# Optimization experiments

Hardware: AMD Instinct MI355X
Metric: run time of the kernel (lower is better)

The kernel has to match this reference:

```python
import jax, jax.numpy as jnp
import numpy as np

L = 248      # max_clip_seq_len
WIN = 3      # window_size
H = 8        # attention heads
D = 768      # input/output dim
HID = 256    # rope hidden dim
SIGMA = 2.0
EPS_LN = 1e-5


def _layernorm(x, g, b):
    m = jnp.mean(x, axis=-1, keepdims=True)
    v = jnp.var(x, axis=-1, keepdims=True)
    return (x - m) / jnp.sqrt(v + EPS_LN) * g + b


def _normalize(x):
    n = jnp.linalg.norm(x, axis=-1, keepdims=True)
    return x / jnp.maximum(n, 1e-12)


def _peb_forward(word_feat, text_feat_full, word_pos, ctx_W, ctx_b, in_W, in_b,
                 out_W, out_b, cn_g, cn_b, r1_W, r1_b, ln_g, ln_b, r2_W, r2_b,
                 pos_emb, pos_temp):
    B, N, _ = word_feat.shape
    valid = word_pos != -1                              # [B,N] bool
    vf = valid.astype(word_feat.dtype)[..., None]       # [B,N,1]
    wp = jnp.clip(word_pos, 0, L - 1)                   # [B,N]
    half = WIN // 2
    offs = jnp.arange(-half, half + 1)
    positions = jnp.clip(wp[..., None] + offs[None, None, :], 0, L - 1)
    ctx = text_feat_full[jnp.arange(B)[:, None, None], positions]
    ctx_anchor = (ctx.reshape(B, N, WIN * D) @ ctx_W + ctx_b) * vf       # [B,N,D]
    q = word_feat * vf                                  # word_proj is Identity (768->768)
    # MultiheadAttention (batch_first), query=q, key=value=ctx_anchor
    hd = D // H
    qp = (q @ in_W[:, :D] + in_b[:D]).reshape(B, N, H, hd)
    kp = (ctx_anchor @ in_W[:, D:2 * D] + in_b[D:2 * D]).reshape(B, N, H, hd)
    vp = (ctx_anchor @ in_W[:, 2 * D:] + in_b[2 * D:]).reshape(B, N, H, hd)
    scores = jnp.einsum('bqhd,bkhd->bhqk', qp, kp) / jnp.sqrt(jnp.asarray(hd, q.dtype))
    attn = jax.nn.softmax(scores, axis=-1)
    ao = jnp.einsum('bhqk,bkhd->bqhd', attn, vp).reshape(B, N, D)
    attn_out = ao @ out_W + out_b
    x = _layernorm(q + attn_out, cn_g, cn_b) * vf       # word_feat_with_ctx
    # rope_mapping: Linear -> GELU -> LayerNorm -> Linear
    rope = _layernorm(jax.nn.gelu(x @ r1_W + r1_b, approximate=False), ln_g, ln_b) @ r2_W + r2_b
    rope_n = _normalize(rope)
    clip_ref_n = _normalize(pos_emb)                    # [L,D]
    temp = jnp.maximum(pos_temp, 0.001)
    logits = jnp.einsum('bnd,ld->bnl', rope_n, clip_ref_n) / temp
    log_q = jax.nn.log_softmax(logits, axis=-1)
    # gaussian soft target over L positions
    pos_idx = jnp.arange(L, dtype=jnp.float32)
    d2 = (pos_idx[None, None, :] - wp[..., None].astype(jnp.float32)) ** 2
    targ = jnp.exp(-d2 / (2.0 * SIGMA ** 2))
    targ = targ / (targ.sum(axis=-1, keepdims=True) + 1e-12)
    lqv = log_q * vf
    tv = targ * vf
    n_valid = valid.sum().astype(jnp.float32)
    safe_t = jnp.where(tv > 0, tv, 1.0)
    kl = jnp.sum(jnp.where(tv > 0, tv * (jnp.log(safe_t) - lqv), 0.0)) / (n_valid + 1e-12)
    # relative position loss on cosine similarity
    pos_sim01 = (jnp.einsum('bnd,bmd->bnm', rope_n, rope_n) + 1.0) / 2.0
    wpf = wp.astype(jnp.float32)
    target_sim = 1.0 - jnp.abs(wpf[:, :, None] - wpf[:, None, :]) / float(L)
    vm2 = vf[:, :, 0][:, None, :] * vf[:, :, 0][:, :, None]
    rel = jnp.sum((pos_sim01 * vm2 - target_sim * vm2) ** 2) / (vm2.sum() + 1e-12)
    peb_loss = (1.0 * kl + 0.5 * rel) * 1.0             # kl_weight=1, rel_weight=0.5, peb_weight=1
    # scatter blended positional features to 248-length sequence (vectorized over batch)
    vals = 0.8 * pos_emb[wp] + 0.2 * rope               # [B,N,D]
    pos_s = jnp.where(valid, wp, L)                     # invalid -> OOB index, dropped
    emb = jnp.zeros((B, L, D), word_feat.dtype).at[jnp.arange(B)[:, None], pos_s].set(vals, mode='drop')
    return emb, peb_loss, kl, rel


def setup_inputs() -> dict:
    key = jax.random.key(0)
    ks = jax.random.split(key, 20)
    B, N = 128, 128
    word_feat = jax.random.normal(ks[0], (B, N, D), jnp.float32)
    text_feat_full = jax.random.normal(ks[1], (B, L, D), jnp.float32)
    # unique sorted positions per batch (scatter is then deterministic, matching torch)
    perms = jax.vmap(lambda k: jax.random.permutation(k, L))(jax.random.split(ks[2], B))
    word_pos = jnp.sort(perms[:, :N], axis=-1).astype(jnp.int32)
    s = 0.02
    return {
        'word_feat': word_feat,
        'text_feat_full': text_feat_full,
        'word_pos': word_pos,
        'ctx_W': s * jax.random.normal(ks[3], (WIN * D, D), jnp.float32),
        'ctx_b': s * jax.random.normal(ks[4], (D,), jnp.float32),
        'in_W': s * jax.random.normal(ks[5], (D, 3 * D), jnp.float32),
        'in_b': s * jax.random.normal(ks[6], (3 * D,), jnp.float32),
        'out_W': s * jax.random.normal(ks[7], (D, D), jnp.float32),
        'out_b': s * jax.random.normal(ks[8], (D,), jnp.float32),
        'cn_g': jnp.ones((D,), jnp.float32) + s * jax.random.normal(ks[9], (D,), jnp.float32),
        'cn_b': s * jax.random.normal(ks[10], (D,), jnp.float32),
        'r1_W': s * jax.random.normal(ks[11], (D, HID), jnp.float32),
        'r1_b': s * jax.random.normal(ks[12], (HID,), jnp.float32),
        'ln_g': jnp.ones((HID,), jnp.float32) + s * jax.random.normal(ks[13], (HID,), jnp.float32),
        'ln_b': s * jax.random.normal(ks[14], (HID,), jnp.float32),
        'r2_W': s * jax.random.normal(ks[15], (HID, D), jnp.float32),
        'r2_b': s * jax.random.normal(ks[16], (D,), jnp.float32),
        'pos_emb': jax.random.normal(ks[17], (L, D), jnp.float32),
        'pos_temp': jnp.asarray(1.0, jnp.float32),
    }


def reference(word_feat, text_feat_full, word_pos, ctx_W, ctx_b, in_W, in_b,
              out_W, out_b, cn_g, cn_b, r1_W, r1_b, ln_g, ln_b, r2_W, r2_b,
              pos_emb, pos_temp):
    return _peb_forward(word_feat, text_feat_full, word_pos, ctx_W, ctx_b, in_W, in_b,
                        out_W, out_b, cn_g, cn_b, r1_W, r1_b, ln_g, ln_b, r2_W, r2_b,
                        pos_emb, pos_temp)
```

## Files before the change

### kernel.cpp

```cpp
#include <hip/hip_runtime.h>
#include <math.h>

#define BB   128
#define NN   128
#define LL   248
#define DD   768
#define HH   8
#define HDh  96
#define HIDN 256
#define MROWS (BB*NN)
#define MB_   (1u<<20)
#define KVLD 1536

typedef unsigned short u16;
typedef unsigned int   u32;
typedef __attribute__((ext_vector_type(8))) short s16x8;
typedef __attribute__((ext_vector_type(4))) float f32x4;

__device__ __forceinline__ u16 f2bf(float x) {
    u32 u = __float_as_uint(x);
    u32 r = u + 0x7fffu + ((u >> 16) & 1u);
    return (u16)(r >> 16);
}
__device__ __forceinline__ float bf2f(u16 h) {
    return __uint_as_float(((u32)h) << 16);
}
__device__ __forceinline__ void gload16(const void* g, void* l) {
    __builtin_amdgcn_global_load_lds(
        (const __attribute__((address_space(1))) void*)g,
        (__attribute__((address_space(3))) void*)l, 16, 0, 0);
}

template<int NT>
__device__ __forceinline__ float breduce_sum(float v, float* red) {
    const int tid = threadIdx.x;
    red[tid] = v; __syncthreads();
#pragma unroll
    for (int o = NT / 2; o > 0; o >>= 1) {
        if (tid < o) red[tid] += red[tid + o];
        __syncthreads();
    }
    float r = red[0]; __syncthreads();
    return r;
}
__device__ __forceinline__ double breduce_sum_d256(double v, double* red) {
    const int tid = threadIdx.x;
    red[tid] = v; __syncthreads();
#pragma unroll
    for (int o = 128; o > 0; o >>= 1) {
        if (tid < o) red[tid] += red[tid + o];
        __syncthreads();
    }
    double r = red[0]; __syncthreads();
    return r;
}

__global__ __launch_bounds__(256)
void transposeAll_kernel(const float* __restrict__ ctx_W, u16* __restrict__ ctx_Wt,
                         const float* __restrict__ in_W,  u16* __restrict__ in_Wt,
                         const float* __restrict__ out_W, u16* __restrict__ out_Wt,
                         const float* __restrict__ r1_W,  u16* __restrict__ r1_Wt,
                         const float* __restrict__ r2_W,  u16* __restrict__ r2_Wt) {
    __shared__ float t[32][33];
    int bid = blockIdx.x;
    const float* src; u16* dst; int R, C;
    if (bid < 1728)      { src = ctx_W; dst = ctx_Wt; R = 2304; C = 768;  }
    else if (bid < 3456) { src = in_W;  dst = in_Wt;  R = 768;  C = 2304; bid -= 1728; }
    else if (bid < 4032) { src = out_W; dst = out_Wt; R = 768;  C = 768;  bid -= 3456; }
    else if (bid < 4224) { src = r1_W;  dst = r1_Wt;  R = 768;  C = 256;  bid -= 4032; }
    else                 { src = r2_W;  dst = r2_Wt;  R = 256;  C = 768;  bid -= 4224; }
    const int ct = C >> 5;
    const int r0 = (bid / ct) * 32, c0 = (bid % ct) * 32;
    const int tx = threadIdx.x & 31, ty = threadIdx.x >> 5;
#pragma unroll
    for (int i = 0; i < 32; i += 8)
        t[ty + i][tx] = src[(size_t)(r0 + ty + i) * C + c0 + tx];
    __syncthreads();
#pragma unroll
    for (int i = 0; i < 32; i += 8)
        dst[(size_t)(c0 + ty + i) * R + r0 + tx] = f2bf(t[tx][ty + i]);
}

#define TEXT_N8 (BB*LL*DD/8)
#define Q_N8    (MROWS*(DD/8))
__global__ __launch_bounds__(256)
void prep_elem_kernel(const float* __restrict__ text, u16* __restrict__ textb,
                      const float* __restrict__ wf, u16* __restrict__ qb,
                      const int* __restrict__ wpos, int* __restrict__ cpos) {
    const int TOT = TEXT_N8 + Q_N8 + MROWS;
    int i = blockIdx.x * 256 + threadIdx.x;
    const int stride = gridDim.x * 256;
    for (; i < TOT; i += stride) {
        if (i < TEXT_N8) {
            const float4* s = (const float4*)(text + (size_t)i * 8);
            float4 a = s[0], b = s[1];
            uint4 o;
            o.x = (u32)f2bf(a.x) | ((u32)f2bf(a.y) << 16);
            o.y = (u32)f2bf(a.z) | ((u32)f2bf(a.w) << 16);
            o.z = (u32)f2bf(b.x) | ((u32)f2bf(b.y) << 16);
            o.w = (u32)f2bf(b.z) | ((u32)f2bf(b.w) << 16);
            *(uint4*)(textb + (size_t)i * 8) = o;
        } else if (i < TEXT_N8 + Q_N8) {
            int c = i - TEXT_N8;
            int row = c / 96;
            float vf = (wpos[row] != -1) ? 1.f : 0.f;
            const float4* s = (const float4*)(wf + (size_t)c * 8);
            float4 a = s[0], b = s[1];
            uint4 o;
            o.x = (u32)f2bf(a.x * vf) | ((u32)f2bf(a.y * vf) << 16);
            o.y = (u32)f2bf(a.z * vf) | ((u32)f2bf(a.w * vf) << 16);
            o.z = (u32)f2bf(b.x * vf) | ((u32)f2bf(b.y * vf) << 16);
            o.w = (u32)f2bf(b.z * vf) | ((u32)f2bf(b.w * vf) << 16);
            *(uint4*)(qb + (size_t)c * 8) = o;
        } else {
            int r = i - TEXT_N8 - Q_N8;
            int w = wpos[r];
            cpos[r] = w < 0 ? 0 : (w > LL - 1 ? LL - 1 : w);
        }
    }
}

__global__ __launch_bounds__(256)
void clipb_kernel(const float* __restrict__ pe, u16* __restrict__ clipb) {
    __shared__ float red[256];
    const int l = blockIdx.x, tid = threadIdx.x;
    if (l >= LL) {
        for (int j = 0; j < 3; ++j)
            clipb[(size_t)l * DD + tid + j * 256] = 0;
        return;
    }
    float t[3]; float q = 0.f;
#pragma unroll
    for (int j = 0; j < 3; ++j) {
        t[j] = pe[(size_t)l * DD + tid + j * 256];
        q = fmaf(t[j], t[j], q);
    }
    q = breduce_sum<256>(q, red);
    float inv = 1.f / fmaxf(sqrtf(q), 1e-12f);
#pragma unroll
    for (int j = 0; j < 3; ++j)
        clipb[(size_t)l * DD + tid + j * 256] = f2bf(t[j] * inv);
}

__device__ __forceinline__ void gemm_step(
    const u16* ga0, const u16* ga1, const u16* gb0, const u16* gb1,
    u16* Ad0, u16* Ad1, u16* Bd0, u16* Bd1,
    const u16* Alds, const u16* Blds,
    const int* aoff, const int* boff, f32x4 acc[4][4]) {
    gload16(ga0, Ad0); gload16(ga1, Ad1);
    gload16(gb0, Bd0); gload16(gb1, Bd1);
    __syncthreads();
    s16x8 af[4], bf[4];
#pragma unroll
    for (int m = 0; m < 4; ++m) af[m] = *(const s16x8*)(Alds + aoff[m]);
#pragma unroll
    for (int n = 0; n < 4; ++n) bf[n] = *(const s16x8*)(Blds + boff[n]);
#pragma unroll
    for (int m = 0; m < 4; ++m)
#pragma unroll
        for (int n = 0; n < 4; ++n)
            acc[m][n] = __builtin_amdgcn_mfma_f32_16x16x32_bf16(
                af[m], bf[n], acc[m][n], 0, 0, 0);
    __syncthreads();
}

template<int GATHER, int CBF16, int MASK>
__global__ __launch_bounds__(256)
void gemm_bt(const u16* __restrict__ A,
             const u16* __restrict__ TXT,
             const int* __restrict__ cpos,
             const u16* __restrict__ Bt,
             const float* __restrict__ bias,
             void* __restrict__ Cout, int ldc, int K,
             const int* __restrict__ wpos) {
    __shared__ __align__(16) u16 Alds[128 * 32];
    __shared__ __align__(16) u16 Blds[128 * 32];
    const int tid = threadIdx.x;
    const int l = tid & 63, wv = tid >> 6;

    const int gx  = gridDim.x;
    const int hw  = blockIdx.y * gx + blockIdx.x;
    const int nwg = gx * gridDim.y;
    const int cpx = nwg >> 3;
    const int lin = (hw & 7) * cpx + (hw >> 3);
    const int m0 = (lin / gx) * 128, n0 = (lin % gx) * 128;

    const int f0 = wv * 1024 + l * 16;
    const int f1 = f0 + 4096;
    const int rA0 = f0 >> 6, rA1 = f1 >> 6;
    const int cb0 = (f0 & 63) ^ (((rA0 >> 1) & 3) << 4);
    const int cb1 = (f1 & 63) ^ (((rA1 >> 1) & 3) << 4);
    const int c0e = cb0 >> 1, c1e = cb1 >> 1;

    u16* Ad0 = Alds + wv * 512;
    u16* Ad1 = Alds + 2048 + wv * 512;
    u16* Bd0 = Blds + wv * 512;
    u16* Bd1 = Blds + 2048 + wv * 512;

    const u16* pb0 = Bt + (size_t)(n0 + rA0) * K + c0e;
    const u16* pb1 = Bt + (size_t)(n0 + rA1) * K + c1e;

    const int wm = (wv >> 1) * 64, wn = (wv & 1) * 64;
    const int la = l & 15, lg = l >> 4;

    int aoff[4], boff[4];
#pragma unroll
    for (int m = 0; m < 4; ++m) {
        int ra = wm + m * 16 + la;
        aoff[m] = ra * 32 + ((lg * 8) ^ (((ra >> 1) & 3) << 3));
        int rb = wn + m * 16 + la;
        boff[m] = rb * 32 + ((lg * 8) ^ (((rb >> 1) & 3) << 3));
    }

    f32x4 acc[4][4] = {};

    if constexpr (GATHER) {
        const int g0 = m0 + rA0, g1 = m0 + rA1;
        const int gb0 = g0 >> 7, gb1 = g1 >> 7;
        const int gc0 = cpos[g0], gc1 = cpos[g1];
#pragma unroll 1
        for (int w = 0; w < 3; ++w) {
            int p0 = gc0 + w - 1; p0 = p0 < 0 ? 0 : (p0 > LL - 1 ? LL - 1 : p0);
            int p1 = gc1 + w - 1; p1 = p1 < 0 ? 0 : (p1 > LL - 1 ? LL - 1 : p1);
            const u16* a0 = TXT + ((size_t)(gb0 * LL + p0)) * DD + c0e;
            const u16* a1 = TXT + ((size_t)(gb1 * LL + p1)) * DD + c1e;
            const u16* b0 = pb0 + w * DD;
            const u16* b1 = pb1 + w * DD;
#pragma unroll 1
            for (int kt = 0; kt < 24; ++kt)
                gemm_step(a0 + kt * 32, a1 + kt * 32, b0 + kt * 32, b1 + kt * 32,
                          Ad0, Ad1, Bd0, Bd1, Alds, Blds, aoff, boff, acc);
        }
    } else {
        const u16* pa0 = A + (size_t)(m0 + rA0) * K + c0e;
        const u16* pa1 = A + (size_t)(m0 + rA1) * K + c1e;
        const int nk = K >> 5;
#pragma unroll 1
        for (int kt = 0; kt < nk; ++kt)
            gemm_step(pa0 + (kt << 5), pa1 + (kt << 5), pb0 + (kt << 5), pb1 + (kt << 5),
                      Ad0, Ad1, Bd0, Bd1, Alds, Blds, aoff, boff, acc);
    }

#pragma unroll
    for (int m = 0; m < 4; ++m) {
        const int rb = m0 + wm + m * 16 + lg * 4;
        float vf[4];
        if constexpr (MASK) {
#pragma unroll
            for (int r = 0; r < 4; ++r) vf[r] = (wpos[rb + r] != -1) ? 1.f : 0.f;
        }
#pragma unroll
        for (int n = 0; n < 4; ++n) {
            const int col = n0 + wn + n * 16 + la;
            const float bv = bias[col];
#pragma unroll
            for (int r = 0; r < 4; ++r) {
                float o = acc[m][n][r] + bv;
                if constexpr (MASK) o *= vf[r];
                if constexpr (CBF16)
                    ((u16*)Cout)[(size_t)(rb + r) * ldc + col] = f2bf(o);
                else
                    ((float*)Cout)[(size_t)(rb + r) * ldc + col] = o;
            }
        }
    }
}

__global__ __launch_bounds__(512)
void attn_mfma_kernel(const u16* __restrict__ qp, const u16* __restrict__ kvb,
                      u16* __restrict__ ao) {
    __shared__ __align__(16) u16 K_lds[128 * 96];
    __shared__ __align__(16) u16 Vt_lds[96 * 128];
    __shared__ __align__(16) u16 P_lds[128 * 128];
    const int bh = blockIdx.x;
    const int b = bh >> 3, h = bh & 7;
    const int tid = threadIdx.x;
    const int l = tid & 63, wv = tid >> 6;
    const int la = l & 15, lg = l >> 4;
    const float scale = 0.10206207261596575f;

    const size_t qbase  = ((size_t)b * NN) * DD + h * HDh;
    const size_t kvbase = ((size_t)b * NN) * KVLD + h * HDh;

#pragma unroll
    for (int i = 0; i < 3; ++i) {
        int f = i * 8192 + wv * 1024 + l * 16;
        int row = f / 192;
        int inner = f - row * 192;
        gload16((const char*)(kvb + kvbase + (size_t)row * KVLD) + inner,
                (char*)K_lds + f);
    }

    uint4 vchunk[3]; int vkey[3], vd0[3];
#pragma unroll
    for (int i = 0; i < 3; ++i) {
        int c = tid + i * 512;
        int key = c / 12, dc = c - key * 12;
        vkey[i] = key; vd0[i] = dc * 8;
        vchunk[i] = *(const uint4*)(kvb + kvbase + (size_t)key * KVLD + DD + dc * 8);
    }

    const int q0 = wv * 16;
    s16x8 qf[3];
#pragma unroll
    for (int kt = 0; kt < 3; ++kt)
        qf[kt] = *(const s16x8*)(qp + qbase + (size_t)(q0 + la) * DD + kt * 32 + lg * 8);

#pragma unroll
    for (int i = 0; i < 3; ++i) {
        const u16* e = (const u16*)&vchunk[i];
#pragma unroll
        for (int j = 0; j < 8; ++j) {
            int d = vd0[i] + j;
            int byte = ((d * 128 + vkey[i]) * 2) ^ ((d & 7) << 4);
            *(u16*)((char*)Vt_lds + byte) = e[j];
        }
    }
    __syncthreads();

    f32x4 sacc[8] = {};
#pragma unroll
    for (int kt = 0; kt < 3; ++kt) {
#pragma unroll
        for (int nf = 0; nf < 8; ++nf) {
            s16x8 bfr = *(const s16x8*)(K_lds + (nf * 16 + la) * 96 + kt * 32 + lg * 8);
            sacc[nf] = __builtin_amdgcn_mfma_f32_16x16x32_bf16(qf[kt], bfr, sacc[nf], 0, 0, 0);
        }
    }

#pragma unroll
    for (int r = 0; r < 4; ++r) {
        float m = -1e30f;
#pragma unroll
        for (int nf = 0; nf < 8; ++nf) m = fmaxf(m, sacc[nf][r]);
#pragma unroll
        for (int o = 8; o > 0; o >>= 1) m = fmaxf(m, __shfl_xor(m, o, 64));
        m *= scale;
        float p[8]; float s = 0.f;
#pragma unroll
        for (int nf = 0; nf < 8; ++nf) { p[nf] = expf(sacc[nf][r] * scale - m); s += p[nf]; }
#pragma unroll
        for (int o = 8; o > 0; o >>= 1) s += __shfl_xor(s, o, 64);
        const float inv = 1.f / s;
        const int q = q0 + lg * 4 + r;
#pragma unroll
        for (int nf = 0; nf < 8; ++nf) {
            int byte = ((q * 128 + nf * 16 + la) * 2) ^ ((q & 7) << 4);
            *(u16*)((char*)P_lds + byte) = f2bf(p[nf] * inv);
        }
    }
    __syncthreads();

    f32x4 oacc[6] = {};
#pragma unroll
    for (int kk = 0; kk < 4; ++kk) {
        const int qrow = q0 + la;
        int abyte = ((qrow * 128 + kk * 32 + lg * 8) * 2) ^ ((qrow & 7) << 4);
        s16x8 af = *(const s16x8*)((char*)P_lds + abyte);
#pragma unroll
        for (int nf = 0; nf < 6; ++nf) {
            const int d = nf * 16 + la;
            int bbyte = ((d * 128 + kk * 32 + lg * 8) * 2) ^ ((d & 7) << 4);
            s16x8 bfr = *(const s16x8*)((char*)Vt_lds + bbyte);
            oacc[nf] = __builtin_amdgcn_mfma_f32_16x16x32_bf16(af, bfr, oacc[nf], 0, 0, 0);
        }
    }

#pragma unroll
    for (int nf = 0; nf < 6; ++nf) {
#pragma unroll
        for (int r = 0; r < 4; ++r) {
            const int q = q0 + lg * 4 + r;
            ao[qbase + (size_t)q * DD + nf * 16 + la] = f2bf(oacc[nf][r]);
        }
    }
}

__global__ __launch_bounds__(256)
void ln768_kernel(const u16* __restrict__ qb, const u16* __restrict__ at,
                  const int* __restrict__ wpos, const float* __restrict__ g,
                  const float* __restrict__ bta, u16* __restrict__ xout) {
    __shared__ float red[256];
    const int r = blockIdx.x, tid = threadIdx.x;
    const float vf = (wpos[r] != -1) ? 1.f : 0.f;
    float t[3]; float s = 0.f, q = 0.f;
#pragma unroll
    for (int j = 0; j < 3; ++j) {
        int d = tid + j * 256;
        t[j] = bf2f(qb[(size_t)r * DD + d]) + bf2f(at[(size_t)r * DD + d]);
        s += t[j];
        q = fmaf(t[j], t[j], q);
    }
    s = breduce_sum<256>(s, red);
    q = breduce_sum<256>(q, red);
    float mean = s * (1.f / DD);
    float var  = q * (1.f / DD) - mean * mean;
    float inv  = 1.f / sqrtf(var + 1e-5f);
#pragma unroll
    for (int j = 0; j < 3; ++j) {
        int d = tid + j * 256;
        xout[(size_t)r * DD + d] = f2bf(((t[j] - mean) * inv * g[d] + bta[d]) * vf);
    }
}

__global__ __launch_bounds__(256)
void ln256_gelu_kernel(const float* __restrict__ g1, const float* __restrict__ lg,
                       const float* __restrict__ lb, u16* __restrict__ hout) {
    __shared__ float red[256];
    const int r = blockIdx.x, tid = threadIdx.x;
    float v  = g1[(size_t)r * HIDN + tid];
    float ge = 0.5f * v * (1.f + erff(v * 0.7071067811865475f));
    float s = breduce_sum<256>(ge, red);
    float q = breduce_sum<256>(ge * ge, red);
    float mean = s * (1.f / HIDN);
    float var  = q * (1.f / HIDN) - mean * mean;
    float inv  = 1.f / sqrtf(var + 1e-5f);
    hout[(size_t)r * HIDN + tid] = f2bf((ge - mean) * inv * lg[tid] + lb[tid]);
}

__global__ __launch_bounds__(256)
void norm_scatter_kernel(const u16* __restrict__ ropeb, const float* __restrict__ pe,
                         const int* __restrict__ wpos, u16* __restrict__ rnb,
                         float* __restrict__ emb) {
    __shared__ float red[256];
    const int r = blockIdx.x, tid = threadIdx.x;
    float t[3]; float q = 0.f;
#pragma unroll
    for (int j = 0; j < 3; ++j) {
        t[j] = bf2f(ropeb[(size_t)r * DD + tid + j * 256]);
        q = fmaf(t[j], t[j], q);
    }
    q = breduce_sum<256>(q, red);
    float inv = 1.f / fmaxf(sqrtf(q), 1e-12f);
    const int wr = wpos[r];
    const bool valid = (wr != -1);
    const int wp = wr < 0 ? 0 : (wr > LL - 1 ? LL - 1 : wr);
    const int b = r >> 7;
#pragma unroll
    for (int j = 0; j < 3; ++j) {
        int d = tid + j * 256;
        rnb[(size_t)r * DD + d] = f2bf(t[j] * inv);
        if (valid)
            emb[((size_t)b * LL + wp) * DD + d] =
                0.8f * pe[(size_t)wp * DD + d] + 0.2f * t[j];
    }
}

__global__ __launch_bounds__(256)
void kl_lite_kernel(const float* __restrict__ logits, const int* __restrict__ wpos,
                    const float* __restrict__ pos_temp, float* __restrict__ klp) {
    const int row = blockIdx.x * 4 + (threadIdx.x >> 6);
    const int l = threadIdx.x & 63;
    const float invt = 1.f / fmaxf(pos_temp[0], 0.001f);
    const float* lrow = logits + (size_t)row * 256;

    float lg[4];
#pragma unroll
    for (int q = 0; q < 4; ++q) {
        int c = l + q * 64;
        lg[q] = (c < LL) ? lrow[c] * invt : -1e30f;
    }
    float m = fmaxf(fmaxf(lg[0], lg[1]), fmaxf(lg[2], lg[3]));
#pragma unroll
    for (int o = 32; o > 0; o >>= 1) m = fmaxf(m, __shfl_xor(m, o, 64));

    float S = 0.f;
#pragma unroll
    for (int q = 0; q < 4; ++q) S += expf(lg[q] - m);
#pragma unroll
    for (int o = 32; o > 0; o >>= 1) S += __shfl_xor(S, o, 64);
    const float logZ = m + logf(S);

    const int wr = wpos[row];
    const bool valid = (wr != -1);
    const int wp = wr < 0 ? 0 : (wr > LL - 1 ? LL - 1 : wr);

    float targ[4]; float tsum = 0.f;
#pragma unroll
    for (int q = 0; q < 4; ++q) {
        int c = l + q * 64;
        float dl = (float)c - (float)wp;
        targ[q] = (c < LL) ? expf(-dl * dl * 0.125f) : 0.f;
        tsum += targ[q];
    }
#pragma unroll
    for (int o = 32; o > 0; o >>= 1) tsum += __shfl_xor(tsum, o, 64);
    const float tden = 1.f / (tsum + 1e-12f);

    float c_ = 0.f;
#pragma unroll
    for (int q = 0; q < 4; ++q) {
        float tn = targ[q] * tden;
        if (valid && tn > 0.f) c_ += tn * (logf(tn) - (lg[q] - logZ));
    }
#pragma unroll
    for (int o = 32; o > 0; o >>= 1) c_ += __shfl_xor(c_, o, 64);
    if (l == 0) klp[row] = c_;
}

__global__ __launch_bounds__(512)
void rel_mfma_kernel(const u16* __restrict__ rnb, const int* __restrict__ wpos,
                     float* __restrict__ rel_part, float* __restrict__ vm2_part) {
    __shared__ __align__(16) u16 T[128 * 32];
    __shared__ float red[512];
    const int blk = blockIdx.x;
    const int b = blk >> 1, jh = blk & 1;
    const int tid = threadIdx.x;
    const int l = tid & 63, wv = tid >> 6;
    const int la = l & 15, lg = l >> 4;

    const int f = wv * 1024 + l * 16;
    const int rA = f >> 6;
    const int cb = (f & 63) ^ (((rA >> 1) & 3) << 4);
    const int ce = cb >> 1;
    const u16* src = rnb + ((size_t)(b * NN + rA)) * DD + ce;
    u16* dst = T + wv * 512;

    const int ra = wv * 16 + la;
    const int aoff = ra * 32 + ((lg * 8) ^ (((ra >> 1) & 3) << 3));
    int boff[4];
#pragma unroll
    for (int nf = 0; nf < 4; ++nf) {
        int rb = jh * 64 + nf * 16 + la;
        boff[nf] = rb * 32 + ((lg * 8) ^ (((rb >> 1) & 3) << 3));
    }

    f32x4 acc[4] = {};
    for (int kt = 0; kt < 24; ++kt) {
        gload16(src + kt * 32, dst);
        __syncthreads();
        s16x8 a = *(const s16x8*)(T + aoff);
        s16x8 bf_[4];
#pragma unroll
        for (int nf = 0; nf < 4; ++nf) bf_[nf] = *(const s16x8*)(T + boff[nf]);
#pragma unroll
        for (int nf = 0; nf < 4; ++nf)
            acc[nf] = __builtin_amdgcn_mfma_f32_16x16x32_bf16(a, bf_[nf], acc[nf], 0, 0, 0);
        __syncthreads();
    }

    float wif[4], vi[4];
#pragma unroll
    for (int r = 0; r < 4; ++r) {
        int wi = wpos[b * NN + wv * 16 + lg * 4 + r];
        vi[r] = (wi != -1) ? 1.f : 0.f;
        wif[r] = (float)(wi < 0 ? 0 : (wi > LL - 1 ? LL - 1 : wi));
    }
    float csum = 0.f, msum = 0.f;
#pragma unroll
    for (int nf = 0; nf < 4; ++nf) {
        int wj = wpos[b * NN + jh * 64 + nf * 16 + la];
        float vj = (wj != -1) ? 1.f : 0.f;
        float wjf = (float)(wj < 0 ? 0 : (wj > LL - 1 ? LL - 1 : wj));
#pragma unroll
        for (int r = 0; r < 4; ++r) {
            float sim = (acc[nf][r] + 1.f) * 0.5f;
            float ts  = 1.f - fabsf(wif[r] - wjf) * (1.f / (float)LL);
            float m2  = vi[r] * vj;
            float df  = m2 * (sim - ts);
            csum += df * df;
            msum += m2;
        }
    }
    csum = breduce_sum<512>(csum, red);
    msum = breduce_sum<512>(msum, red);
    if (tid == 0) { rel_part[blk] = csum; vm2_part[blk] = msum; }
}

__global__ __launch_bounds__(256)
void final_kernel(const float* __restrict__ klp, const float* __restrict__ relp,
                  const float* __restrict__ vmp, const int* __restrict__ wpos,
                  float* __restrict__ outs) {
    __shared__ double rd[256];
    const int tid = threadIdx.x;
    double kl = 0.0, rel = 0.0, vm = 0.0, nv = 0.0;
    for (int r = tid; r < MROWS; r += 256) {
        kl += (double)klp[r];
        nv += (wpos[r] != -1) ? 1.0 : 0.0;
    }
    if (tid < 256) {
        rel += (double)relp[tid];
        vm  += (double)vmp[tid];
    }
    kl  = breduce_sum_d256(kl, rd);
    rel = breduce_sum_d256(rel, rd);
    vm  = breduce_sum_d256(vm, rd);
    nv  = breduce_sum_d256(nv, rd);
    if (tid == 0) {
        float klf  = (float)(kl / (nv + 1e-12));
        float relf = (float)(rel / (vm + 1e-12));
        outs[0] = klf + 0.5f * relf;
        outs[1] = klf;
        outs[2] = relf;
    }
}

extern "C" void kernel_launch(void* const* d_in, const int* in_sizes, int n_in,
                              void* d_out, int out_size, void* d_ws, size_t ws_size,
                              hipStream_t stream) {
    (void)in_sizes; (void)n_in; (void)ws_size;

    const float* word_feat = (const float*)d_in[0];
    const float* text      = (const float*)d_in[1];
    const int*   wpos      = (const int*)d_in[2];
    const float* ctx_W     = (const float*)d_in[3];
    const float* ctx_b     = (const float*)d_in[4];
    const float* in_W      = (const float*)d_in[5];
    const float* in_b      = (const float*)d_in[6];
    const float* out_W     = (const float*)d_in[7];
    const float* out_b     = (const float*)d_in[8];
    const float* cn_g      = (const float*)d_in[9];
    const float* cn_b      = (const float*)d_in[10];
    const float* r1_W      = (const float*)d_in[11];
    const float* r1_b      = (const float*)d_in[12];
    const float* ln_g      = (const float*)d_in[13];
    const float* ln_b      = (const float*)d_in[14];
    const float* r2_W      = (const float*)d_in[15];
    const float* r2_b      = (const float*)d_in[16];
    const float* pos_emb   = (const float*)d_in[17];
    const float* pos_temp  = (const float*)d_in[18];

    char* W = (char*)d_ws;
    u16*   ctx_Wt = (u16*)(W);
    u16*   in_Wt  = ctx_Wt + (size_t)768 * 2304;
    u16*   out_Wt = in_Wt  + (size_t)2304 * 768;
    u16*   r1_Wt  = out_Wt + (size_t)768 * 768;
    u16*   r2_Wt  = r1_Wt  + (size_t)256 * 768;
    u16*   clipb  = r2_Wt + (size_t)768 * 256;
    int*   cposb  = (int*)(clipb + (size_t)256 * DD);
    float* klp    = (float*)(cposb + MROWS);
    float* relp   = klp + MROWS;
    float* vmp    = relp + 256;
    float* zbias  = vmp + 256;
    u16*   textb  = (u16*)(W + (size_t)12 * MB_);
    u16*   atoutb = textb;
    float* logits = (float*)(W + (size_t)12 * MB_);
    u16*   xb     = (u16*)(W + (size_t)36 * MB_);
    u16*   qb     = (u16*)(W + (size_t)60 * MB_);
    u16*   ctxa   = (u16*)(W + (size_t)86 * MB_);
    u16*   aob    = ctxa;
    u16*   rnb    = ctxa;
    u16*   qpb    = (u16*)(W + (size_t)112 * MB_);
    float* g1     = (float*)(W + (size_t)112 * MB_);
    u16*   hb     = (u16*)(W + (size_t)128 * MB_);
    u16*   kvb    = (u16*)(W + (size_t)138 * MB_);
    u16*   ropeb  = kvb;

    hipMemsetAsync(d_out, 0, (size_t)out_size * sizeof(float), stream);
    hipMemsetAsync(zbias, 0, 256 * sizeof(float), stream);

    dim3 blk(256);

    transposeAll_kernel<<<dim3(4416), blk, 0, stream>>>(
        ctx_W, ctx_Wt, in_W, in_Wt, out_W, out_Wt, r1_W, r1_Wt, r2_W, r2_Wt);
    prep_elem_kernel<<<dim3(2048), blk, 0, stream>>>(
        text, textb, word_feat, qb, wpos, cposb);
    clipb_kernel<<<dim3(256), blk, 0, stream>>>(pos_emb, clipb);

    dim3 g768(6, 128);
    dim3 g1536(12, 128);
    dim3 g256(2, 128);

    gemm_bt<1, 1, 1><<<g768, blk, 0, stream>>>(
        nullptr, textb, cposb, ctx_Wt, ctx_b, ctxa, DD, 3 * DD, wpos);
    gemm_bt<0, 1, 0><<<g768, blk, 0, stream>>>(
        qb, nullptr, nullptr, in_Wt, in_b, qpb, DD, DD, nullptr);
    gemm_bt<0, 1, 0><<<g1536, blk, 0, stream>>>(
        ctxa, nullptr, nullptr, in_Wt + (size_t)768 * 768, in_b + DD, kvb, KVLD, DD, nullptr);
    attn_mfma_kernel<<<dim3(BB * HH), dim3(512), 0, stream>>>(qpb, kvb, aob);
    gemm_bt<0, 1, 0><<<g768, blk, 0, stream>>>(
        aob, nullptr, nullptr, out_Wt, out_b, atoutb, DD, DD, nullptr);
    ln768_kernel<<<dim3(MROWS), blk, 0, stream>>>(qb, atoutb, wpos, cn_g, cn_b, xb);
    gemm_bt<0, 0, 0><<<g256, blk, 0, stream>>>(
        xb, nullptr, nullptr, r1_Wt, r1_b, g1, HIDN, DD, nullptr);
    ln256_gelu_kernel<<<dim3(MROWS), blk, 0, stream>>>(g1, ln_g, ln_b, hb);
    gemm_bt<0, 1, 0><<<g768, blk, 0, stream>>>(
        hb, nullptr, nullptr, r2_Wt, r2_b, ropeb, DD, HIDN, nullptr);
    norm_scatter_kernel<<<dim3(MROWS), blk, 0, stream>>>(
        ropeb, pos_emb, wpos, rnb, (float*)d_out);
    gemm_bt<0, 0, 0><<<g256, blk, 0, stream>>>(
        rnb, nullptr, nullptr, clipb, zbias, logits, 256, DD, nullptr);
    kl_lite_kernel<<<dim3(MROWS / 4), blk, 0, stream>>>(logits, wpos, pos_temp, klp);
    rel_mfma_kernel<<<dim3(BB * 2), dim3(512), 0, stream>>>(rnb, wpos, relp, vmp);
    final_kernel<<<dim3(1), blk, 0, stream>>>(
        klp, relp, vmp, wpos, (float*)d_out + (size_t)BB * LL * DD);
}
```

Measured before the change: 454.8 us.

## Double GEMM K-tile to 64 with XOR swizzle and merge prep kernels

The bf16 MFMA GEMM now stages a K depth of 64 per step instead of 32. Each thread loads four 16-byte rows into a 64-wide shared-memory tile that uses a new XOR chunk swizzle, and runs two MFMA sub-steps per tile. This halves the number of barrier-separated load/compute rounds. It doubles shared memory per block to 32 KB, which may lower occupancy. Separately, the weight-transpose, element-conversion and clip-normalise prep kernels are merged into one launch that dispatches on block index, saving launch gaps.

```diff
diff --git a/kernel.cpp b/kernel.cpp
--- a/kernel.cpp
+++ b/kernel.cpp
@@ -55,113 +55,91 @@
     return r;
 }
 
-__global__ __launch_bounds__(256)
-void transposeAll_kernel(const float* __restrict__ ctx_W, u16* __restrict__ ctx_Wt,
-                         const float* __restrict__ in_W,  u16* __restrict__ in_Wt,
-                         const float* __restrict__ out_W, u16* __restrict__ out_Wt,
-                         const float* __restrict__ r1_W,  u16* __restrict__ r1_Wt,
-                         const float* __restrict__ r2_W,  u16* __restrict__ r2_Wt) {
-    __shared__ float t[32][33];
-    int bid = blockIdx.x;
-    const float* src; u16* dst; int R, C;
-    if (bid < 1728)      { src = ctx_W; dst = ctx_Wt; R = 2304; C = 768;  }
-    else if (bid < 3456) { src = in_W;  dst = in_Wt;  R = 768;  C = 2304; bid -= 1728; }
-    else if (bid < 4032) { src = out_W; dst = out_Wt; R = 768;  C = 768;  bid -= 3456; }
-    else if (bid < 4224) { src = r1_W;  dst = r1_Wt;  R = 768;  C = 256;  bid -= 4032; }
-    else                 { src = r2_W;  dst = r2_Wt;  R = 256;  C = 768;  bid -= 4224; }
-    const int ct = C >> 5;
-    const int r0 = (bid / ct) * 32, c0 = (bid % ct) * 32;
-    const int tx = threadIdx.x & 31, ty = threadIdx.x >> 5;
-#pragma unroll
-    for (int i = 0; i < 32; i += 8)
-        t[ty + i][tx] = src[(size_t)(r0 + ty + i) * C + c0 + tx];
-    __syncthreads();
-#pragma unroll
-    for (int i = 0; i < 32; i += 8)
-        dst[(size_t)(c0 + ty + i) * R + r0 + tx] = f2bf(t[tx][ty + i]);
-}
-
 #define TEXT_N8 (BB*LL*DD/8)
 #define Q_N8    (MROWS*(DD/8))
 __global__ __launch_bounds__(256)
-void prep_elem_kernel(const float* __restrict__ text, u16* __restrict__ textb,
-                      const float* __restrict__ wf, u16* __restrict__ qb,
-                      const int* __restrict__ wpos, int* __restrict__ cpos) {
-    const int TOT = TEXT_N8 + Q_N8 + MROWS;
-    int i = blockIdx.x * 256 + threadIdx.x;
-    const int stride = gridDim.x * 256;
-    for (; i < TOT; i += stride) {
-        if (i < TEXT_N8) {
-            const float4* s = (const float4*)(text + (size_t)i * 8);
-            float4 a = s[0], b = s[1];
-            uint4 o;
-            o.x = (u32)f2bf(a.x) | ((u32)f2bf(a.y) << 16);
-            o.y = (u32)f2bf(a.z) | ((u32)f2bf(a.w) << 16);
-            o.z = (u32)f2bf(b.x) | ((u32)f2bf(b.y) << 16);
-            o.w = (u32)f2bf(b.z) | ((u32)f2bf(b.w) << 16);
-            *(uint4*)(textb + (size_t)i * 8) = o;
-        } else if (i < TEXT_N8 + Q_N8) {
-            int c = i - TEXT_N8;
-            int row = c / 96;
-            float vf = (wpos[row] != -1) ? 1.f : 0.f;
-            const float4* s = (const float4*)(wf + (size_t)c * 8);
-            float4 a = s[0], b = s[1];
-            uint4 o;
-            o.x = (u32)f2bf(a.x * vf) | ((u32)f2bf(a.y * vf) << 16);
-            o.y = (u32)f2bf(a.z * vf) | ((u32)f2bf(a.w * vf) << 16);
-            o.z = (u32)f2bf(b.x * vf) | ((u32)f2bf(b.y * vf) << 16);
-            o.w = (u32)f2bf(b.z * vf) | ((u32)f2bf(b.w * vf) << 16);
-            *(uint4*)(qb + (size_t)c * 8) = o;
-        } else {
-            int r = i - TEXT_N8 - Q_N8;
-            int w = wpos[r];
-            cpos[r] = w < 0 ? 0 : (w > LL - 1 ? LL - 1 : w);
-        }
-    }
-}
-
-__global__ __launch_bounds__(256)
-void clipb_kernel(const float* __restrict__ pe, u16* __restrict__ clipb) {
-    __shared__ float red[256];
-    const int l = blockIdx.x, tid = threadIdx.x;
-    if (l >= LL) {
+void prep_all_kernel(const float* __restrict__ ctx_W, u16* __restrict__ ctx_Wt,
+                     const float* __restrict__ in_W,  u16* __restrict__ in_Wt,
+                     const float* __restrict__ out_W, u16* __restrict__ out_Wt,
+                     const float* __restrict__ r1_W,  u16* __restrict__ r1_Wt,
+                     const float* __restrict__ r2_W,  u16* __restrict__ r2_Wt,
+                     const float* __restrict__ text,  u16* __restrict__ textb,
+                     const float* __restrict__ wf,    u16* __restrict__ qb,
+                     const int* __restrict__ wpos,    int* __restrict__ cpos,
+                     const float* __restrict__ pe,    u16* __restrict__ clipb) {
+    __shared__ float smem[32 * 33];
+    int bid = blockIdx.x;
+    const int tid = threadIdx.x;
+
+    if (bid < 4416) {
+        const float* src; u16* dst; int C;
+        if (bid < 1728)      { src = ctx_W; dst = ctx_Wt; C = 768;  }
+        else if (bid < 3456) { src = in_W;  dst = in_Wt;  C = 2304; bid -= 1728; }
+        else if (bid < 4032) { src = out_W; dst = out_Wt; C = 768;  bid -= 3456; }
+        else if (bid < 4224) { src = r1_W;  dst = r1_Wt;  C = 256;  bid -= 4032; }
+        else                 { src = r2_W;  dst = r2_Wt;  C = 768;  bid -= 4224; }
+        const int R = (C == 768) ? ((dst == ctx_Wt) ? 2304 : ((dst == out_Wt) ? 768 : 256))
+                                 : ((C == 2304) ? 768 : 768);
+        const int ct = C >> 5;
+        const int r0 = (bid / ct) * 32, c0 = (bid % ct) * 32;
+        const int tx = tid & 31, ty = tid >> 5;
+#pragma unroll
+        for (int i = 0; i < 32; i += 8)
+            smem[(ty + i) * 33 + tx] = src[(size_t)(r0 + ty + i) * C + c0 + tx];
+        __syncthreads();
+#pragma unroll
+        for (int i = 0; i < 32; i += 8)
+            dst[(size_t)(c0 + ty + i) * R + r0 + tx] = f2bf(smem[tx * 33 + ty + i]);
+    } else if (bid < 4672) {
+        const int l = bid - 4416;
+        if (l >= LL) {
+            for (int j = 0; j < 3; ++j) clipb[(size_t)l * DD + tid + j * 256] = 0;
+            return;
+        }
+        float t[3]; float q = 0.f;
+#pragma unroll
+        for (int j = 0; j < 3; ++j) {
+            t[j] = pe[(size_t)l * DD + tid + j * 256];
+            q = fmaf(t[j], t[j], q);
+        }
+        q = breduce_sum<256>(q, smem);
+        float inv = 1.f / fmaxf(sqrtf(q), 1e-12f);
+#pragma unroll
         for (int j = 0; j < 3; ++j)
-            clipb[(size_t)l * DD + tid + j * 256] = 0;
-        return;
-    }
-    float t[3]; float q = 0.f;
-#pragma unroll
-    for (int j = 0; j < 3; ++j) {
-        t[j] = pe[(size_t)l * DD + tid + j * 256];
-        q = fmaf(t[j], t[j], q);
-    }
-    q = breduce_sum<256>(q, red);
-    float inv = 1.f / fmaxf(sqrtf(q), 1e-12f);
-#pragma unroll
-    for (int j = 0; j < 3; ++j)
-        clipb[(size_t)l * DD + tid + j * 256] = f2bf(t[j] * inv);
-}
-
-__device__ __forceinline__ void gemm_step(
-    const u16* ga0, const u16* ga1, const u16* gb0, const u16* gb1,
-    u16* Ad0, u16* Ad1, u16* Bd0, u16* Bd1,
-    const u16* Alds, const u16* Blds,
-    const int* aoff, const int* boff, f32x4 acc[4][4]) {
-    gload16(ga0, Ad0); gload16(ga1, Ad1);
-    gload16(gb0, Bd0); gload16(gb1, Bd1);
-    __syncthreads();
-    s16x8 af[4], bf[4];
-#pragma unroll
-    for (int m = 0; m < 4; ++m) af[m] = *(const s16x8*)(Alds + aoff[m]);
-#pragma unroll
-    for (int n = 0; n < 4; ++n) bf[n] = *(const s16x8*)(Blds + boff[n]);
-#pragma unroll
-    for (int m = 0; m < 4; ++m)
-#pragma unroll
-        for (int n = 0; n < 4; ++n)
-            acc[m][n] = __builtin_amdgcn_mfma_f32_16x16x32_bf16(
-                af[m], bf[n], acc[m][n], 0, 0, 0);
-    __syncthreads();
+            clipb[(size_t)l * DD + tid + j * 256] = f2bf(t[j] * inv);
+    } else {
+        const int TOT = TEXT_N8 + Q_N8 + MROWS;
+        int i = (bid - 4672) * 256 + tid;
+        const int stride = 2048 * 256;
+        for (; i < TOT; i += stride) {
+            if (i < TEXT_N8) {
+                const float4* s = (const float4*)(text + (size_t)i * 8);
+                float4 a = s[0], b = s[1];
+                uint4 o;
+                o.x = (u32)f2bf(a.x) | ((u32)f2bf(a.y) << 16);
+                o.y = (u32)f2bf(a.z) | ((u32)f2bf(a.w) << 16);
+                o.z = (u32)f2bf(b.x) | ((u32)f2bf(b.y) << 16);
+                o.w = (u32)f2bf(b.z) | ((u32)f2bf(b.w) << 16);
+                *(uint4*)(textb + (size_t)i * 8) = o;
+            } else if (i < TEXT_N8 + Q_N8) {
+                int c = i - TEXT_N8;
+                int row = c / 96;
+                float vf = (wpos[row] != -1) ? 1.f : 0.f;
+                const float4* s = (const float4*)(wf + (size_t)c * 8);
+                float4 a = s[0], b = s[1];
+                uint4 o;
+                o.x = (u32)f2bf(a.x * vf) | ((u32)f2bf(a.y * vf) << 16);
+                o.y = (u32)f2bf(a.z * vf) | ((u32)f2bf(a.w * vf) << 16);
+                o.z = (u32)f2bf(b.x * vf) | ((u32)f2bf(b.y * vf) << 16);
+                o.w = (u32)f2bf(b.z * vf) | ((u32)f2bf(b.w * vf) << 16);
+                *(uint4*)(qb + (size_t)c * 8) = o;
+            } else {
+                int r = i - TEXT_N8 - Q_N8;
+                int w = wpos[r];
+                cpos[r] = w < 0 ? 0 : (w > LL - 1 ? LL - 1 : w);
+            }
+        }
+    }
 }
 
 template<int GATHER, int CBF16, int MASK>
@@ -173,8 +151,8 @@
              const float* __restrict__ bias,
              void* __restrict__ Cout, int ldc, int K,
              const int* __restrict__ wpos) {
-    __shared__ __align__(16) u16 Alds[128 * 32];
-    __shared__ __align__(16) u16 Blds[128 * 32];
+    __shared__ __align__(16) u16 Alds[128 * 64];
+    __shared__ __align__(16) u16 Blds[128 * 64];
     const int tid = threadIdx.x;
     const int l = tid & 63, wv = tid >> 6;
 
@@ -185,20 +163,10 @@
     const int lin = (hw & 7) * cpx + (hw >> 3);
     const int m0 = (lin / gx) * 128, n0 = (lin % gx) * 128;
 
-    const int f0 = wv * 1024 + l * 16;
-    const int f1 = f0 + 4096;
-    const int rA0 = f0 >> 6, rA1 = f1 >> 6;
-    const int cb0 = (f0 & 63) ^ (((rA0 >> 1) & 3) << 4);
-    const int cb1 = (f1 & 63) ^ (((rA1 >> 1) & 3) << 4);
-    const int c0e = cb0 >> 1, c1e = cb1 >> 1;
-
+    const int rw = wv * 8 + (l >> 3);
+    const int ce = ((l & 7) ^ (l >> 3)) << 3;
     u16* Ad0 = Alds + wv * 512;
-    u16* Ad1 = Alds + 2048 + wv * 512;
     u16* Bd0 = Blds + wv * 512;
-    u16* Bd1 = Blds + 2048 + wv * 512;
-
-    const u16* pb0 = Bt + (size_t)(n0 + rA0) * K + c0e;
-    const u16* pb1 = Bt + (size_t)(n0 + rA1) * K + c1e;
 
     const int wm = (wv >> 1) * 64, wn = (wv & 1) * 64;
     const int la = l & 15, lg = l >> 4;
@@ -207,38 +175,81 @@
 #pragma unroll
     for (int m = 0; m < 4; ++m) {
         int ra = wm + m * 16 + la;
-        aoff[m] = ra * 32 + ((lg * 8) ^ (((ra >> 1) & 3) << 3));
+        aoff[m] = ra * 64 + (((lg ^ (la & 7)) << 3));
         int rb = wn + m * 16 + la;
-        boff[m] = rb * 32 + ((lg * 8) ^ (((rb >> 1) & 3) << 3));
-    }
+        boff[m] = rb * 64 + (((lg ^ (la & 7)) << 3));
+    }
+
+    const u16* pb[4];
+#pragma unroll
+    for (int i = 0; i < 4; ++i)
+        pb[i] = Bt + (size_t)(n0 + rw + i * 32) * K + ce;
 
     f32x4 acc[4][4] = {};
 
+    auto do_step = [&](const u16* a0, const u16* a1, const u16* a2, const u16* a3,
+                       const u16* b0, const u16* b1, const u16* b2, const u16* b3) {
+        gload16(a0, Ad0);
+        gload16(a1, Ad0 + 2048);
+        gload16(a2, Ad0 + 4096);
+        gload16(a3, Ad0 + 6144);
+        gload16(b0, Bd0);
+        gload16(b1, Bd0 + 2048);
+        gload16(b2, Bd0 + 4096);
+        gload16(b3, Bd0 + 6144);
+        __syncthreads();
+#pragma unroll
+        for (int kk = 0; kk < 2; ++kk) {
+            const int kx = kk << 5;
+            s16x8 af[4], bf[4];
+#pragma unroll
+            for (int m = 0; m < 4; ++m) af[m] = *(const s16x8*)(Alds + (aoff[m] ^ kx));
+#pragma unroll
+            for (int n = 0; n < 4; ++n) bf[n] = *(const s16x8*)(Blds + (boff[n] ^ kx));
+#pragma unroll
+            for (int m = 0; m < 4; ++m)
+#pragma unroll
+                for (int n = 0; n < 4; ++n)
+                    acc[m][n] = __builtin_amdgcn_mfma_f32_16x16x32_bf16(
+                        af[m], bf[n], acc[m][n], 0, 0, 0);
+        }
+        __syncthreads();
+    };
+
     if constexpr (GATHER) {
-        const int g0 = m0 + rA0, g1 = m0 + rA1;
-        const int gb0 = g0 >> 7, gb1 = g1 >> 7;
-        const int gc0 = cpos[g0], gc1 = cpos[g1];
+        int gb[4], gc[4];
+#pragma unroll
+        for (int i = 0; i < 4; ++i) {
+            int g = m0 + rw + i * 32;
+            gb[i] = g >> 7;
+            gc[i] = cpos[g];
+        }
 #pragma unroll 1
         for (int w = 0; w < 3; ++w) {
-            int p0 = gc0 + w - 1; p0 = p0 < 0 ? 0 : (p0 > LL - 1 ? LL - 1 : p0);
-            int p1 = gc1 + w - 1; p1 = p1 < 0 ? 0 : (p1 > LL - 1 ? LL - 1 : p1);
-            const u16* a0 = TXT + ((size_t)(gb0 * LL + p0)) * DD + c0e;
-            const u16* a1 = TXT + ((size_t)(gb1 * LL + p1)) * DD + c1e;
-            const u16* b0 = pb0 + w * DD;
-            const u16* b1 = pb1 + w * DD;
+            const u16* pa[4];
+#pragma unroll
+            for (int i = 0; i < 4; ++i) {
+                int p = gc[i] + w - 1;
+                p = p < 0 ? 0 : (p > LL - 1 ? LL - 1 : p);
+                pa[i] = TXT + ((size_t)(gb[i] * LL + p)) * DD + ce;
+            }
+            const u16* b0 = pb[0] + w * DD; const u16* b1 = pb[1] + w * DD;
+            const u16* b2 = pb[2] + w * DD; const u16* b3 = pb[3] + w * DD;
 #pragma unroll 1
-            for (int kt = 0; kt < 24; ++kt)
-                gemm_step(a0 + kt * 32, a1 + kt * 32, b0 + kt * 32, b1 + kt * 32,
-                          Ad0, Ad1, Bd0, Bd1, Alds, Blds, aoff, boff, acc);
+            for (int kt = 0; kt < 12; ++kt)
+                do_step(pa[0] + kt * 64, pa[1] + kt * 64, pa[2] + kt * 64, pa[3] + kt * 64,
+                        b0 + kt * 64, b1 + kt * 64, b2 + kt * 64, b3 + kt * 64);
         }
     } else {
-        const u16* pa0 = A + (size_t)(m0 + rA0) * K + c0e;
-        const u16* pa1 = A + (size_t)(m0 + rA1) * K + c1e;
-        const int nk = K >> 5;
+        const u16* pa[4];
+#pragma unroll
+        for (int i = 0; i < 4; ++i)
+            pa[i] = A + (size_t)(m0 + rw + i * 32) * K + ce;
+        const int nk = K >> 6;
 #pragma unroll 1
         for (int kt = 0; kt < nk; ++kt)
-            gemm_step(pa0 + (kt << 5), pa1 + (kt << 5), pb0 + (kt << 5), pb1 + (kt << 5),
-                      Ad0, Ad1, Bd0, Bd1, Alds, Blds, aoff, boff, acc);
+            do_step(pa[0] + kt * 64, pa[1] + kt * 64, pa[2] + kt * 64, pa[3] + kt * 64,
+                    pb[0] + kt * 64, pb[1] + kt * 64, pb[2] + kt * 64, pb[3] + kt * 64);
     }
 
 #pragma unroll
@@ -651,11 +662,9 @@
 
     dim3 blk(256);
 
-    transposeAll_kernel<<<dim3(4416), blk, 0, stream>>>(
-        ctx_W, ctx_Wt, in_W, in_Wt, out_W, out_Wt, r1_W, r1_Wt, r2_W, r2_Wt);
-    prep_elem_kernel<<<dim3(2048), blk, 0, stream>>>(
-        text, textb, word_feat, qb, wpos, cposb);
-    clipb_kernel<<<dim3(256), blk, 0, stream>>>(pos_emb, clipb);
+    prep_all_kernel<<<dim3(4416 + 256 + 2048), blk, 0, stream>>>(
+        ctx_W, ctx_Wt, in_W, in_Wt, out_W, out_Wt, r1_W, r1_Wt, r2_W, r2_Wt,
+        text, textb, word_feat, qb, wpos, cposb, pos_emb, clipb);
 
     dim3 g768(6, 128);
     dim3 g1536(12, 128);
```

Measured after the change: 447.5 us. No clear change (-1.6%).
